# Optimization experiments

Hardware: AMD Instinct MI355X
Metric: run time of the kernel (lower is better)

Reference implementation:

```python
import jax, jax.numpy as jnp
import numpy as np

ATTN = 128

def _gelu(x):
    return jax.nn.gelu(x, approximate=False)

def _mlp3(x, W1, b1, W2, b2, W3, b3):
    h = _gelu(x @ W1.T + b1)
    h = _gelu(h @ W2.T + b2)
    return h @ W3.T + b3

def setup_inputs() -> dict:
    key = jax.random.key(0)
    ks = jax.random.split(key, 32)
    B, K, M, C = 128, 64, 2048, 32
    QD, AD, H = 128, 128, 256
    s = 0.02
    d = {}
    d['g'] = jax.random.normal(ks[0], (B, K, 3), dtype=jnp.float32)
    d['query'] = jax.random.normal(ks[1], (M, QD), dtype=jnp.float32) * s
    d['qW'] = jax.random.normal(ks[2], (AD, QD), dtype=jnp.float32) * s
    d['qb'] = jnp.zeros((AD,), jnp.float32)
    d['kW'] = jax.random.normal(ks[3], (AD, 1), dtype=jnp.float32) * s
    d['kb'] = jnp.zeros((AD,), jnp.float32)
    # global_mlp: K -> H -> H -> H
    d['gm_W1'] = jax.random.normal(ks[4], (H, K), dtype=jnp.float32) * s
    d['gm_b1'] = jnp.zeros((H,), jnp.float32)
    d['gm_W2'] = jax.random.normal(ks[5], (H, H), dtype=jnp.float32) * s
    d['gm_b2'] = jnp.zeros((H,), jnp.float32)
    d['gm_W3'] = jax.random.normal(ks[6], (H, H), dtype=jnp.float32) * s
    d['gm_b3'] = jnp.zeros((H,), jnp.float32)
    # point_mlp: (H+QD+1) -> H -> H -> H
    d['pm_W1'] = jax.random.normal(ks[7], (H, H + QD + 1), dtype=jnp.float32) * s
    d['pm_b1'] = jnp.zeros((H,), jnp.float32)
    d['pm_W2'] = jax.random.normal(ks[8], (H, H), dtype=jnp.float32) * s
    d['pm_b2'] = jnp.zeros((H,), jnp.float32)
    d['pm_W3'] = jax.random.normal(ks[9], (H, H), dtype=jnp.float32) * s
    d['pm_b3'] = jnp.zeros((H,), jnp.float32)
    d['tW'] = jax.random.normal(ks[10], (C, H), dtype=jnp.float32) * s
    d['tb'] = jnp.zeros((C,), jnp.float32)
    d['wW'] = jax.random.normal(ks[11], (1, H), dtype=jnp.float32) * s
    d['wb'] = jnp.zeros((1,), jnp.float32)
    d['cW'] = jax.random.normal(ks[12], (1, H), dtype=jnp.float32) * s
    d['cb'] = jnp.zeros((1,), jnp.float32)
    return d

def reference(g, query, qW, qb, kW, kb,
              gm_W1, gm_b1, gm_W2, gm_b2, gm_W3, gm_b3,
              pm_W1, pm_b1, pm_W2, pm_b2, pm_W3, pm_b3,
              tW, tb, wW, wb, cW, cb):
    B, K, _ = g.shape
    M = query.shape[0]
    inv = jnp.linalg.norm(g, axis=-1)                    # (B,K)
    Q = query @ qW.T + qb                                # (M,AD)
    Kk = inv[..., None] * kW[:, 0] + kb                  # (B,K,AD) Linear(1->AD)
    scores = jnp.einsum('md,bkd->bmk', Q, Kk) / jnp.sqrt(jnp.float32(Q.shape[-1]))
    A = jax.nn.softmax(scores, axis=-1)                  # (B,M,K)
    y = jnp.einsum('bmk,bkd->bmd', A, g)                 # (B,M,3)
    global_s = _mlp3(inv, gm_W1, gm_b1, gm_W2, gm_b2, gm_W3, gm_b3)  # (B,H)
    attended_inv = jnp.einsum('bmk,bk->bm', A, inv)      # (B,M)
    s_in = jnp.concatenate([
        jnp.broadcast_to(global_s[:, None, :], (B, M, global_s.shape[-1])),
        jnp.broadcast_to(query[None], (B, M, query.shape[-1])),
        attended_inv[..., None],
    ], axis=-1)                                          # (B,M,H+QD+1)
    s = _mlp3(s_in, pm_W1, pm_b1, pm_W2, pm_b2, pm_W3, pm_b3)  # (B,M,H)
    type_logits = s @ tW.T + tb                          # (B,M,C)
    weight_logits = (s @ wW.T + wb)[..., 0]              # (B,M)
    gate = jnp.clip(jax.nn.sigmoid(s @ cW.T + cb), 0.0, 1.0)  # (B,M,1)
    y = y * gate
    return (y, type_logits, weight_logits)
```

## Files before the change

kernel.cpp:

```cpp
#include <hip/hip_runtime.h>
#include <hip/hip_bf16.h>
#include <math.h>


typedef __attribute__((ext_vector_type(8))) short short8;
typedef __attribute__((ext_vector_type(4))) float f32x4;
typedef __attribute__((ext_vector_type(16))) float f32x16;

__device__ __forceinline__ unsigned short bf16_rne(float f){
    union { float f; unsigned u; } v; v.f = f;
    return (unsigned short)((v.u + 0x7FFFu + ((v.u >> 16) & 1u)) >> 16);
}
__device__ __forceinline__ unsigned pk_bf16(float a, float b){
    float2 t; t.x = a; t.y = b;
    __hip_bfloat162 h = __float22bfloat162_rn(t);
    union { __hip_bfloat162 h; unsigned u; } cv; cv.h = h;
    return cv.u;
}
__device__ __forceinline__ short8 cvt8_f4(const float* __restrict__ p){
    float4 a = *(const float4*)p;
    float4 b = *(const float4*)(p + 4);
    short8 s;
    s[0]=(short)bf16_rne(a.x); s[1]=(short)bf16_rne(a.y);
    s[2]=(short)bf16_rne(a.z); s[3]=(short)bf16_rne(a.w);
    s[4]=(short)bf16_rne(b.x); s[5]=(short)bf16_rne(b.y);
    s[6]=(short)bf16_rne(b.z); s[7]=(short)bf16_rne(b.w);
    return s;
}

__device__ __forceinline__ float gelu_f(float x){
    float z  = x * 0.70710678118654752f;
    float az = fabsf(z);
    float t  = __builtin_amdgcn_rcpf(1.0f + 0.3275911f * az);
    float p  = t*(0.254829592f + t*(-0.284496736f + t*(1.421413741f + t*(-1.453152027f + t*1.061405429f))));
    float e  = __expf(-az*az);
    float er = copysignf(1.0f - p*e, z);
    return 0.5f * x * (1.0f + er);
}
__device__ __forceinline__ float gelu_poly(float x){
    float t = x*x;
    float p = fmaf(t, -2.9761905e-3f, 2.5e-2f);
    p = fmaf(t, p, -0.16666667f);
    p = fmaf(t, p, 1.0f);
    float Phi = fmaf(x*p, 0.39894228f, 0.5f);
    Phi = fminf(fmaxf(Phi, 0.0f), 1.0f);
    return x * Phi;
}

__global__ __launch_bounds__(256)
void k_prep(const float* __restrict__ g, const float* __restrict__ qW,
            const float* __restrict__ qb, const float* __restrict__ kW,
            const float* __restrict__ query, const float* __restrict__ pmW1,
            const float* __restrict__ pmb1,
            const float* __restrict__ pmW2, const float* __restrict__ pmW3,
            const float* __restrict__ pmb3,
            const float* __restrict__ gmW1, const float* __restrict__ gmb1,
            const float* __restrict__ gmW2, const float* __restrict__ gmb2,
            const float* __restrict__ gmW3, const float* __restrict__ gmb3,
            const float* __restrict__ tW, const float* __restrict__ tb,
            const float* __restrict__ wW, const float* __restrict__ wb,
            const float* __restrict__ cW, const float* __restrict__ cb,
            float* __restrict__ invg, float* __restrict__ ag,
            float* __restrict__ u1g, float* __restrict__ u2g,
            unsigned short* __restrict__ w2b, unsigned short* __restrict__ wheadb,
            float* __restrict__ bheadg, float* __restrict__ w385g) {
    __shared__ __align__(16) unsigned char smem[87040];
    const int bid = blockIdx.x, tid = threadIdx.x;
    const int w = tid >> 6, lane = tid & 63, q = lane >> 4, ln = lane & 15;

    if (bid < 32) {
        int idx = bid*256 + tid;
        const float* p = g + idx*3;
        invg[idx] = sqrtf(p[0]*p[0] + p[1]*p[1] + p[2]*p[2]);
    } else if (bid < 96) {
        int o = (bid - 32)*1024 + tid*4;
        float4 x = *(const float4*)&pmW2[o];
        union { unsigned short u[4]; uint2 v; } r;
        r.u[0] = bf16_rne(x.x); r.u[1] = bf16_rne(x.y);
        r.u[2] = bf16_rne(x.z); r.u[3] = bf16_rne(x.w);
        *(uint2*)&w2b[o] = r.v;
    } else if (bid < 130) {
        float* hw = (float*)smem;
        int c = bid - 96;
        const float* src = (c < 32) ? (tW + c*256) : ((c == 32) ? wW : cW);
        hw[tid] = src[tid];
        __syncthreads();
        float acc = 0.f;
        for (int j = 0; j < 256; ++j) acc += hw[j] * pmW3[j*256 + tid];
        wheadb[c*256 + tid] = bf16_rne(acc);
        if (tid == 0) {
            float bacc = (c < 32) ? tb[c] : ((c == 32) ? wb[0] : cb[0]);
            for (int j = 0; j < 256; ++j) bacc += hw[j] * pmb3[j];
            bheadg[c] = bacc;
        }
    } else if (bid == 130) {
        w385g[tid] = pmW1[tid*385 + 384];
    } else if (bid < 139) {
        float* kws = (float*)smem;
        float* vs  = kws + 128;
        float* red = vs  + 128;
        if (tid < 128) kws[tid] = kW[tid];
        __syncthreads();
        if (tid < 128) {
            float acc = 0.f;
            for (int d = 0; d < 128; ++d) acc += qW[d*128 + tid] * kws[d];
            vs[tid] = acc;
            red[tid] = qb[tid] * kws[tid];
        }
        __syncthreads();
        float s0 = 0.f;
        #pragma unroll 8
        for (int i = 0; i < 128; ++i) s0 += red[i];
        int m = (bid - 131)*256 + tid;
        const float4* qp = (const float4*)(query + m*128);
        float acc = s0;
        #pragma unroll 8
        for (int e4 = 0; e4 < 32; ++e4) {
            float4 qv = qp[e4];
            acc += qv.x*vs[e4*4] + qv.y*vs[e4*4+1] + qv.z*vs[e4*4+2] + qv.w*vs[e4*4+3];
        }
        ag[m] = acc * 0.08838834764831845f;
    } else if (bid < 141) {
        unsigned short* invA = (unsigned short*)smem;
        unsigned short* hA   = (unsigned short*)(smem + 9216);
        unsigned short* hB   = (unsigned short*)(smem + 43008);
        const int b0 = (bid - 139)*64;
        for (int i = tid; i < 4096; i += 256) {
            int r = i >> 6, k = i & 63;
            const float* p = g + ((size_t)(b0 + r)*64 + k)*3;
            invA[r*72 + k] = bf16_rne(sqrtf(p[0]*p[0] + p[1]*p[1] + p[2]*p[2]));
        }
        __syncthreads();

        f32x4 acc[4][4];
        #pragma unroll
        for (int mt = 0; mt < 4; ++mt)
            #pragma unroll
            for (int nt = 0; nt < 4; ++nt) acc[mt][nt] = (f32x4){0.f,0.f,0.f,0.f};
        #pragma unroll
        for (int kk = 0; kk < 2; ++kk) {
            const int kc = kk*32 + q*8;
            short8 af[4], bf_[4];
            #pragma unroll
            for (int mt = 0; mt < 4; ++mt) af[mt] = *(const short8*)&invA[(mt*16 + ln)*72 + kc];
            #pragma unroll
            for (int nt = 0; nt < 4; ++nt) bf_[nt] = cvt8_f4(gmW1 + (w*64 + nt*16 + ln)*64 + kc);
            #pragma unroll
            for (int mt = 0; mt < 4; ++mt)
                #pragma unroll
                for (int nt = 0; nt < 4; ++nt)
                    acc[mt][nt] = __builtin_amdgcn_mfma_f32_16x16x32_bf16(af[mt], bf_[nt], acc[mt][nt], 0, 0, 0);
        }
        #pragma unroll
        for (int mt = 0; mt < 4; ++mt)
            #pragma unroll
            for (int nt = 0; nt < 4; ++nt) {
                const int n = w*64 + nt*16 + ln;
                const float bb = gmb1[n];
                #pragma unroll
                for (int rg = 0; rg < 4; ++rg)
                    hA[(mt*16 + q*4 + rg)*264 + n] = bf16_rne(gelu_f(acc[mt][nt][rg] + bb));
            }
        __syncthreads();
        #pragma unroll
        for (int mt = 0; mt < 4; ++mt)
            #pragma unroll
            for (int nt = 0; nt < 4; ++nt) acc[mt][nt] = (f32x4){0.f,0.f,0.f,0.f};
        for (int kk = 0; kk < 8; ++kk) {
            const int kc = kk*32 + q*8;
            short8 af[4], bf_[4];
            #pragma unroll
            for (int mt = 0; mt < 4; ++mt) af[mt] = *(const short8*)&hA[(mt*16 + ln)*264 + kc];
            #pragma unroll
            for (int nt = 0; nt < 4; ++nt) bf_[nt] = cvt8_f4(gmW2 + (w*64 + nt*16 + ln)*256 + kc);
            #pragma unroll
            for (int mt = 0; mt < 4; ++mt)
                #pragma unroll
                for (int nt = 0; nt < 4; ++nt)
                    acc[mt][nt] = __builtin_amdgcn_mfma_f32_16x16x32_bf16(af[mt], bf_[nt], acc[mt][nt], 0, 0, 0);
        }
        __syncthreads();
        #pragma unroll
        for (int mt = 0; mt < 4; ++mt)
            #pragma unroll
            for (int nt = 0; nt < 4; ++nt) {
                const int n = w*64 + nt*16 + ln;
                const float bb = gmb2[n];
                #pragma unroll
                for (int rg = 0; rg < 4; ++rg)
                    hB[(mt*16 + q*4 + rg)*264 + n] = bf16_rne(gelu_f(acc[mt][nt][rg] + bb));
            }
        __syncthreads();
        #pragma unroll
        for (int mt = 0; mt < 4; ++mt)
            #pragma unroll
            for (int nt = 0; nt < 4; ++nt) acc[mt][nt] = (f32x4){0.f,0.f,0.f,0.f};
        for (int kk = 0; kk < 8; ++kk) {
            const int kc = kk*32 + q*8;
            short8 af[4], bf_[4];
            #pragma unroll
            for (int mt = 0; mt < 4; ++mt) af[mt] = *(const short8*)&hB[(mt*16 + ln)*264 + kc];
            #pragma unroll
            for (int nt = 0; nt < 4; ++nt) bf_[nt] = cvt8_f4(gmW3 + (w*64 + nt*16 + ln)*256 + kc);
            #pragma unroll
            for (int mt = 0; mt < 4; ++mt)
                #pragma unroll
                for (int nt = 0; nt < 4; ++nt)
                    acc[mt][nt] = __builtin_amdgcn_mfma_f32_16x16x32_bf16(af[mt], bf_[nt], acc[mt][nt], 0, 0, 0);
        }
        __syncthreads();
        #pragma unroll
        for (int mt = 0; mt < 4; ++mt)
            #pragma unroll
            for (int nt = 0; nt < 4; ++nt) {
                const int n = w*64 + nt*16 + ln;
                const float bb = gmb3[n];
                #pragma unroll
                for (int rg = 0; rg < 4; ++rg)
                    hA[(mt*16 + q*4 + rg)*264 + n] = bf16_rne(acc[mt][nt][rg] + bb);
            }
        unsigned short* w1s = (unsigned short*)(smem + 43008);
        #pragma unroll
        for (int mt = 0; mt < 4; ++mt)
            #pragma unroll
            for (int nt = 0; nt < 4; ++nt) acc[mt][nt] = (f32x4){0.f,0.f,0.f,0.f};
        for (int chunk = 0; chunk < 4; ++chunk) {
            __syncthreads();
            for (int i = tid; i < 256*64; i += 256) {
                int n = i >> 6, c = i & 63;
                w1s[n*72 + c] = bf16_rne(pmW1[(size_t)n*385 + chunk*64 + c]);
            }
            __syncthreads();
            #pragma unroll
            for (int kk2 = 0; kk2 < 2; ++kk2) {
                const int kl = kk2*32 + q*8;
                const int kg = chunk*64 + kl;
                short8 af[4], bf_[4];
                #pragma unroll
                for (int mt = 0; mt < 4; ++mt) af[mt] = *(const short8*)&hA[(mt*16 + ln)*264 + kg];
                #pragma unroll
                for (int nt = 0; nt < 4; ++nt) bf_[nt] = *(const short8*)&w1s[(w*64 + nt*16 + ln)*72 + kl];
                #pragma unroll
                for (int mt = 0; mt < 4; ++mt)
                    #pragma unroll
                    for (int nt = 0; nt < 4; ++nt)
                        acc[mt][nt] = __builtin_amdgcn_mfma_f32_16x16x32_bf16(af[mt], bf_[nt], acc[mt][nt], 0, 0, 0);
            }
        }
        #pragma unroll
        for (int mt = 0; mt < 4; ++mt)
            #pragma unroll
            for (int nt = 0; nt < 4; ++nt) {
                const int n = w*64 + nt*16 + ln;
                const float bb = pmb1[n];
                #pragma unroll
                for (int rg = 0; rg < 4; ++rg)
                    u1g[(size_t)(b0 + mt*16 + q*4 + rg)*256 + n] = acc[mt][nt][rg] + bb;
            }
    } else {
        unsigned short* qs = (unsigned short*)smem;
        unsigned short* wsd = (unsigned short*)(smem + 17408);
        const int m0 = (bid - 141)*64;
        for (int i = tid; i < 64*128; i += 256) {
            int r = i >> 7, c = i & 127;
            qs[r*136 + c] = bf16_rne(query[(size_t)(m0 + r)*128 + c]);
        }
        for (int i = tid; i < 256*128; i += 256) {
            int n = i >> 7, c = i & 127;
            wsd[n*136 + c] = bf16_rne(pmW1[(size_t)n*385 + 256 + c]);
        }
        __syncthreads();
        f32x4 acc[4][4];
        #pragma unroll
        for (int mt = 0; mt < 4; ++mt)
            #pragma unroll
            for (int nt = 0; nt < 4; ++nt) acc[mt][nt] = (f32x4){0.f,0.f,0.f,0.f};
        #pragma unroll
        for (int kk = 0; kk < 4; ++kk) {
            const int kc = kk*32 + q*8;
            short8 af[4], bf_[4];
            #pragma unroll
            for (int mt = 0; mt < 4; ++mt) af[mt] = *(const short8*)&qs[(mt*16 + ln)*136 + kc];
            #pragma unroll
            for (int nt = 0; nt < 4; ++nt) bf_[nt] = *(const short8*)&wsd[(w*64 + nt*16 + ln)*136 + kc];
            #pragma unroll
            for (int mt = 0; mt < 4; ++mt)
                #pragma unroll
                for (int nt = 0; nt < 4; ++nt)
                    acc[mt][nt] = __builtin_amdgcn_mfma_f32_16x16x32_bf16(af[mt], bf_[nt], acc[mt][nt], 0, 0, 0);
        }
        #pragma unroll
        for (int mt = 0; mt < 4; ++mt)
            #pragma unroll
            for (int nt = 0; nt < 4; ++nt) {
                const int n = w*64 + nt*16 + ln;
                #pragma unroll
                for (int rg = 0; rg < 4; ++rg)
                    u2g[(size_t)(m0 + mt*16 + q*4 + rg)*256 + n] = acc[mt][nt][rg];
            }
    }
}

__global__ __launch_bounds__(256, 6)
void k_main(const float* __restrict__ g,
            const float* __restrict__ invg, const float* __restrict__ ag,
            const float* __restrict__ u1g, const float* __restrict__ u2g,
            const float* __restrict__ w385g, const float* __restrict__ pmb2,
            const unsigned short* __restrict__ w2b, const unsigned short* __restrict__ wheadb,
            const float* __restrict__ bheadg, float* __restrict__ out) {
    __shared__ __align__(16) unsigned short hb[32*264];
    __shared__ __align__(16) float u1s[256], w385s[256], pmb2s[256];
    __shared__ float invs[64], gsl[192], ainv_s[32], y0s[96];

    const int tid = threadIdx.x;
    const int bid = blockIdx.x;
    const int b  = bid >> 6;
    const int m0 = (bid & 63) << 5;

    if (tid < 64)  invs[tid] = invg[b*64 + tid];
    if (tid < 192) gsl[tid]  = g[b*192 + tid];
    u1s[tid]   = u1g[b*256 + tid];
    w385s[tid] = w385g[tid];
    pmb2s[tid] = pmb2[tid];
    __syncthreads();

    {
        const int r = tid >> 3, sub = tid & 7;
        const float am = ag[m0 + r];
        const int kb = sub * 8;
        float mx = -1e30f;
        #pragma unroll
        for (int i = 0; i < 8; ++i) mx = fmaxf(mx, invs[kb + i] * am);
        #pragma unroll
        for (int d = 1; d < 8; d <<= 1) mx = fmaxf(mx, __shfl_xor(mx, d, 64));
        float den = 0.f, ai = 0.f, y0 = 0.f, y1 = 0.f, y2 = 0.f;
        #pragma unroll
        for (int i = 0; i < 8; ++i) {
            const int k = kb + i;
            const float iv = invs[k];
            const float e = __expf(iv * am - mx);
            den += e; ai += e * iv;
            y0 += e * gsl[k*3+0]; y1 += e * gsl[k*3+1]; y2 += e * gsl[k*3+2];
        }
        #pragma unroll
        for (int d = 1; d < 8; d <<= 1) {
            den += __shfl_xor(den, d, 64);
            ai  += __shfl_xor(ai , d, 64);
            y0  += __shfl_xor(y0 , d, 64);
            y1  += __shfl_xor(y1 , d, 64);
            y2  += __shfl_xor(y2 , d, 64);
        }
        if (sub == 0) {
            const float id = 1.0f / den;
            ainv_s[r] = ai * id;
            y0s[r*3+0] = y0*id; y0s[r*3+1] = y1*id; y0s[r*3+2] = y2*id;
        }
    }
    __syncthreads();

    const int w = tid >> 6, lane = tid & 63;
    const int q = lane >> 4, ln = lane & 15;
    const int h5 = lane >> 5, m31 = lane & 31;

    const unsigned short* w2p = w2b + (size_t)(w*64 + m31)*256 + h5*8;
    short8 acur0 = *(const short8*)(w2p);
    short8 acur1 = *(const short8*)(w2p + 32*256);

    {
        const int ln16 = tid & 15, rbase = tid >> 4;
        #pragma unroll
        for (int rr = 0; rr < 2; ++rr) {
            const int r = rr*16 + rbase;
            const float aiv = ainv_s[r];
            const float* u2p = u2g + (size_t)(m0 + r)*256;
            #pragma unroll
            for (int k = 0; k < 4; ++k) {
                const int c = ln16*4 + k*64;
                float4 x  = *(const float4*)&u2p[c];
                float4 uv = *(const float4*)&u1s[c];
                float4 wv = *(const float4*)&w385s[c];
                float g0 = gelu_poly(x.x + uv.x + aiv*wv.x);
                float g1 = gelu_poly(x.y + uv.y + aiv*wv.y);
                float g2 = gelu_poly(x.z + uv.z + aiv*wv.z);
                float g3 = gelu_poly(x.w + uv.w + aiv*wv.w);
                uint2 pk; pk.x = pk_bf16(g0, g1); pk.y = pk_bf16(g2, g3);
                *(uint2*)&hb[r*264 + c] = pk;
            }
        }
    }
    __syncthreads();

    f32x16 acc2[2];
    #pragma unroll
    for (int a = 0; a < 2; ++a)
        #pragma unroll
        for (int i = 0; i < 16; ++i) acc2[a][i] = 0.f;

    {
        short8 anxt0, anxt1;
        #pragma unroll
        for (int kk = 0; kk < 16; ++kk) {
            if (kk < 15) {
                anxt0 = *(const short8*)(w2p + (kk+1)*16);
                anxt1 = *(const short8*)(w2p + 32*256 + (kk+1)*16);
            }
            const int kc = kk*16 + h5*8;
            short8 b0 = *(const short8*)&hb[m31*264 + kc];
            acc2[0] = __builtin_amdgcn_mfma_f32_32x32x16_bf16(acur0, b0, acc2[0], 0, 0, 0);
            acc2[1] = __builtin_amdgcn_mfma_f32_32x32x16_bf16(acur1, b0, acc2[1], 0, 0, 0);
            acur0 = anxt0; acur1 = anxt1;
        }
    }
    __syncthreads();

    #pragma unroll
    for (int a = 0; a < 2; ++a) {
        #pragma unroll
        for (int gg = 0; gg < 4; ++gg) {
            const int n0 = w*64 + a*32 + gg*8 + h5*4;
            const float4 bb4 = *(const float4*)&pmb2s[n0];
            float h0 = gelu_poly(acc2[a][gg*4+0] + bb4.x);
            float h1 = gelu_poly(acc2[a][gg*4+1] + bb4.y);
            float h2 = gelu_poly(acc2[a][gg*4+2] + bb4.z);
            float h3 = gelu_poly(acc2[a][gg*4+3] + bb4.w);
            uint2 pk2; pk2.x = pk_bf16(h0, h1); pk2.y = pk_bf16(h2, h3);
            *(uint2*)&hb[m31*264 + n0] = pk2;
        }
    }

    const int cb2 = (ln < 2) ? (32 + ln) : 33;
    const unsigned short* whp = wheadb + q*8;
    const bool evenw = ((w & 1) == 0);
    short8 wf0, wf1, wf2;
    if (evenw) {
        wf0 = *(const short8*)(whp +  ln      *256);
        wf1 = *(const short8*)(whp + (16 + ln)*256);
    } else {
        wf2 = *(const short8*)(whp +  cb2     *256);
    }
    __syncthreads();

    const int rr = (w >> 1)*16 + ln;
    f32x4 accA0 = {0.f,0.f,0.f,0.f}, accA1 = {0.f,0.f,0.f,0.f}, accB = {0.f,0.f,0.f,0.f};
    #pragma unroll
    for (int kk = 0; kk < 8; ++kk) {
        short8 wn0, wn1, wn2;
        if (kk < 7) {
            if (evenw) {
                wn0 = *(const short8*)(whp +  ln      *256 + (kk+1)*32);
                wn1 = *(const short8*)(whp + (16 + ln)*256 + (kk+1)*32);
            } else {
                wn2 = *(const short8*)(whp +  cb2     *256 + (kk+1)*32);
            }
        }
        short8 bh = *(const short8*)&hb[rr*264 + kk*32 + q*8];
        if (evenw) {
            accA0 = __builtin_amdgcn_mfma_f32_16x16x32_bf16(wf0, bh, accA0, 0, 0, 0);
            accA1 = __builtin_amdgcn_mfma_f32_16x16x32_bf16(wf1, bh, accA1, 0, 0, 0);
            wf0 = wn0; wf1 = wn1;
        } else {
            accB  = __builtin_amdgcn_mfma_f32_16x16x32_bf16(wf2, bh, accB , 0, 0, 0);
            wf2 = wn2;
        }
    }
    {
        const size_t row = (size_t)b*2048 + m0 + rr;
        const int c0 = q*4;
        if (evenw) {
            f32x4 r0 = accA0 + *(const f32x4*)&bheadg[c0];
            f32x4 r1 = accA1 + *(const f32x4*)&bheadg[16 + c0];
            *(f32x4*)&out[786432 + row*32 + c0]      = r0;
            *(f32x4*)&out[786432 + row*32 + 16 + c0] = r1;
        } else if (q == 0) {
            out[9175040 + row] = accB[0] + bheadg[32];
            float gv = accB[1] + bheadg[33];
            float gt = 1.0f / (1.0f + __expf(-gv));
            gt = fminf(fmaxf(gt, 0.0f), 1.0f);
            float* yo = out + row*3;
            yo[0] = y0s[rr*3+0] * gt;
            yo[1] = y0s[rr*3+1] * gt;
            yo[2] = y0s[rr*3+2] * gt;
        }
    }
}

extern "C" void kernel_launch(void* const* d_in, const int* in_sizes, int n_in,
                              void* d_out, int out_size, void* d_ws, size_t ws_size,
                              hipStream_t stream) {
    const float* g     = (const float*)d_in[0];
    const float* query = (const float*)d_in[1];
    const float* qW    = (const float*)d_in[2];
    const float* qb    = (const float*)d_in[3];
    const float* kW    = (const float*)d_in[4];
    const float* gmW1  = (const float*)d_in[6];
    const float* gmb1  = (const float*)d_in[7];
    const float* gmW2  = (const float*)d_in[8];
    const float* gmb2  = (const float*)d_in[9];
    const float* gmW3  = (const float*)d_in[10];
    const float* gmb3  = (const float*)d_in[11];
    const float* pmW1  = (const float*)d_in[12];
    const float* pmb1  = (const float*)d_in[13];
    const float* pmW2  = (const float*)d_in[14];
    const float* pmb2  = (const float*)d_in[15];
    const float* pmW3  = (const float*)d_in[16];
    const float* pmb3  = (const float*)d_in[17];
    const float* tW    = (const float*)d_in[18];
    const float* tb    = (const float*)d_in[19];
    const float* wW    = (const float*)d_in[20];
    const float* wb    = (const float*)d_in[21];
    const float* cW    = (const float*)d_in[22];
    const float* cb    = (const float*)d_in[23];
    float* out = (float*)d_out;

    float* ws    = (float*)d_ws;
    float* invg  = ws;
    float* ag    = ws + 8192;
    float* u1g   = ws + 10240;
    float* w385g = ws + 43008;
    float* bheadg= ws + 43264;
    unsigned short* w2b    = (unsigned short*)(ws + 43328);
    unsigned short* wheadb = (unsigned short*)(ws + 76096);
    float* u2g   = ws + 80448;

    hipLaunchKernelGGL(k_prep, dim3(173), dim3(256), 0, stream,
                       g, qW, qb, kW, query, pmW1, pmb1, pmW2, pmW3, pmb3,
                       gmW1, gmb1, gmW2, gmb2, gmW3, gmb3,
                       tW, tb, wW, wb, cW, cb,
                       invg, ag, u1g, u2g, w2b, wheadb, bheadg, w385g);
    hipLaunchKernelGGL(k_main, dim3(8192), dim3(256), 0, stream,
                       g, invg, ag, u1g, u2g, w385g, pmb2,
                       w2b, wheadb, bheadg, out);
}
```

Baseline: 314.9 us.

## Make k_main persistent per batch half with W2 resident in LDS

The main kernel now launches 256 blocks of 512 threads. Each block handles one batch element's half of the M rows and loops over 32 tiles of 32 rows. The full bf16 W2 matrix (256x256) is loaded into LDS once per block instead of being streamed from global memory for every 32-row tile. The next tile's u2 rows are prefetched into registers, and the head GEMMs are redistributed over 6 waves. The trade-offs are roughly 135KB of LDS per block, which forces one block per CU, only 256 blocks for the whole GPU, and a serial per-tile loop with several barriers per iteration.

```diff
diff --git a/kernel.cpp b/kernel.cpp
--- a/kernel.cpp
+++ b/kernel.cpp
@@ -301,60 +301,48 @@
     }
 }
 
-__global__ __launch_bounds__(256, 6)
+__global__ __launch_bounds__(512)
 void k_main(const float* __restrict__ g,
             const float* __restrict__ invg, const float* __restrict__ ag,
             const float* __restrict__ u1g, const float* __restrict__ u2g,
             const float* __restrict__ w385g, const float* __restrict__ pmb2,
             const unsigned short* __restrict__ w2b, const unsigned short* __restrict__ wheadb,
             const float* __restrict__ bheadg, float* __restrict__ out) {
+    __shared__ __align__(16) unsigned short w2s[256*264];
     __shared__ __align__(16) unsigned short hb[32*264];
-    __shared__ __align__(16) float u1s[256], w385s[256], pmb2s[256];
-    __shared__ float invs[64], gsl[192], ainv_s[32], y0s[96];
+    __shared__ __align__(16) float u1s[256];
+    __shared__ __align__(16) float w385s[256];
+    __shared__ __align__(16) float pmb2s[256];
+    __shared__ __align__(16) float bheads[36];
+    __shared__ float invs[64], gsl[192], y0s[96];
 
     const int tid = threadIdx.x;
     const int bid = blockIdx.x;
-    const int b  = bid >> 6;
-    const int m0 = (bid & 63) << 5;
+    const int b   = bid >> 1;
+    const int mbase = (bid & 1) << 10;
 
     if (tid < 64)  invs[tid] = invg[b*64 + tid];
     if (tid < 192) gsl[tid]  = g[b*192 + tid];
-    u1s[tid]   = u1g[b*256 + tid];
-    w385s[tid] = w385g[tid];
-    pmb2s[tid] = pmb2[tid];
-    __syncthreads();
-
+    if (tid < 256) {
+        u1s[tid]   = u1g[b*256 + tid];
+        w385s[tid] = w385g[tid];
+        pmb2s[tid] = pmb2[tid];
+    }
+    if (tid < 34) bheads[tid] = bheadg[tid];
+
+    const int r32 = tid >> 4;
+    const int cb  = (tid & 15) << 2;
+    float4 u2r[4];
     {
-        const int r = tid >> 3, sub = tid & 7;
-        const float am = ag[m0 + r];
-        const int kb = sub * 8;
-        float mx = -1e30f;
-        #pragma unroll
-        for (int i = 0; i < 8; ++i) mx = fmaxf(mx, invs[kb + i] * am);
-        #pragma unroll
-        for (int d = 1; d < 8; d <<= 1) mx = fmaxf(mx, __shfl_xor(mx, d, 64));
-        float den = 0.f, ai = 0.f, y0 = 0.f, y1 = 0.f, y2 = 0.f;
-        #pragma unroll
-        for (int i = 0; i < 8; ++i) {
-            const int k = kb + i;
-            const float iv = invs[k];
-            const float e = __expf(iv * am - mx);
-            den += e; ai += e * iv;
-            y0 += e * gsl[k*3+0]; y1 += e * gsl[k*3+1]; y2 += e * gsl[k*3+2];
-        }
-        #pragma unroll
-        for (int d = 1; d < 8; d <<= 1) {
-            den += __shfl_xor(den, d, 64);
-            ai  += __shfl_xor(ai , d, 64);
-            y0  += __shfl_xor(y0 , d, 64);
-            y1  += __shfl_xor(y1 , d, 64);
-            y2  += __shfl_xor(y2 , d, 64);
-        }
-        if (sub == 0) {
-            const float id = 1.0f / den;
-            ainv_s[r] = ai * id;
-            y0s[r*3+0] = y0*id; y0s[r*3+1] = y1*id; y0s[r*3+2] = y2*id;
-        }
+        const float* p = u2g + (size_t)(mbase + r32)*256 + cb;
+        #pragma unroll
+        for (int j = 0; j < 4; ++j) u2r[j] = *(const float4*)(p + j*64);
+    }
+    #pragma unroll
+    for (int j = 0; j < 16; ++j) {
+        int idx = tid + j*512;
+        int n = idx >> 5, c = (idx & 31) << 3;
+        *(short8*)&w2s[n*264 + c] = *(const short8*)&w2b[idx*8];
     }
     __syncthreads();
 
@@ -362,21 +350,43 @@
     const int q = lane >> 4, ln = lane & 15;
     const int h5 = lane >> 5, m31 = lane & 31;
 
-    const unsigned short* w2p = w2b + (size_t)(w*64 + m31)*256 + h5*8;
-    short8 acur0 = *(const short8*)(w2p);
-    short8 acur1 = *(const short8*)(w2p + 32*256);
-
-    {
-        const int ln16 = tid & 15, rbase = tid >> 4;
-        #pragma unroll
-        for (int rr = 0; rr < 2; ++rr) {
-            const int r = rr*16 + rbase;
-            const float aiv = ainv_s[r];
-            const float* u2p = u2g + (size_t)(m0 + r)*256;
-            #pragma unroll
-            for (int k = 0; k < 4; ++k) {
-                const int c = ln16*4 + k*64;
-                float4 x  = *(const float4*)&u2p[c];
+    for (int t = 0; t < 32; ++t) {
+        const int m0 = mbase + t*32;
+
+        {
+            const float am = ag[m0 + r32];
+            const int kb = (tid & 15) * 4;
+            float mx = -1e30f;
+            #pragma unroll
+            for (int i = 0; i < 4; ++i) mx = fmaxf(mx, invs[kb + i] * am);
+            #pragma unroll
+            for (int d = 1; d < 16; d <<= 1) mx = fmaxf(mx, __shfl_xor(mx, d, 64));
+            float den = 0.f, ai = 0.f, y0 = 0.f, y1 = 0.f, y2 = 0.f;
+            #pragma unroll
+            for (int i = 0; i < 4; ++i) {
+                const int k = kb + i;
+                const float iv = invs[k];
+                const float e = __expf(iv * am - mx);
+                den += e; ai += e * iv;
+                y0 += e * gsl[k*3+0]; y1 += e * gsl[k*3+1]; y2 += e * gsl[k*3+2];
+            }
+            #pragma unroll
+            for (int d = 1; d < 16; d <<= 1) {
+                den += __shfl_xor(den, d, 64);
+                ai  += __shfl_xor(ai , d, 64);
+                y0  += __shfl_xor(y0 , d, 64);
+                y1  += __shfl_xor(y1 , d, 64);
+                y2  += __shfl_xor(y2 , d, 64);
+            }
+            const float id = 1.0f / den;
+            const float aiv = ai * id;
+            if ((tid & 15) == 0) {
+                y0s[r32*3+0] = y0*id; y0s[r32*3+1] = y1*id; y0s[r32*3+2] = y2*id;
+            }
+            #pragma unroll
+            for (int j = 0; j < 4; ++j) {
+                const int c = cb + j*64;
+                float4 x  = u2r[j];
                 float4 uv = *(const float4*)&u1s[c];
                 float4 wv = *(const float4*)&w385s[c];
                 float g0 = gelu_poly(x.x + uv.x + aiv*wv.x);
@@ -384,103 +394,95 @@
                 float g2 = gelu_poly(x.z + uv.z + aiv*wv.z);
                 float g3 = gelu_poly(x.w + uv.w + aiv*wv.w);
                 uint2 pk; pk.x = pk_bf16(g0, g1); pk.y = pk_bf16(g2, g3);
-                *(uint2*)&hb[r*264 + c] = pk;
-            }
-        }
-    }
-    __syncthreads();
-
-    f32x16 acc2[2];
-    #pragma unroll
-    for (int a = 0; a < 2; ++a)
-        #pragma unroll
-        for (int i = 0; i < 16; ++i) acc2[a][i] = 0.f;
-
-    {
-        short8 anxt0, anxt1;
-        #pragma unroll
-        for (int kk = 0; kk < 16; ++kk) {
-            if (kk < 15) {
-                anxt0 = *(const short8*)(w2p + (kk+1)*16);
-                anxt1 = *(const short8*)(w2p + 32*256 + (kk+1)*16);
-            }
-            const int kc = kk*16 + h5*8;
-            short8 b0 = *(const short8*)&hb[m31*264 + kc];
-            acc2[0] = __builtin_amdgcn_mfma_f32_32x32x16_bf16(acur0, b0, acc2[0], 0, 0, 0);
-            acc2[1] = __builtin_amdgcn_mfma_f32_32x32x16_bf16(acur1, b0, acc2[1], 0, 0, 0);
-            acur0 = anxt0; acur1 = anxt1;
-        }
-    }
-    __syncthreads();
-
-    #pragma unroll
-    for (int a = 0; a < 2; ++a) {
+                *(uint2*)&hb[r32*264 + c] = pk;
+            }
+        }
+        if (t < 31) {
+            const float* p = u2g + (size_t)(m0 + 32 + r32)*256 + cb;
+            #pragma unroll
+            for (int j = 0; j < 4; ++j) u2r[j] = *(const float4*)(p + j*64);
+        }
+        __syncthreads();
+
+        f32x16 acc;
+        #pragma unroll
+        for (int i = 0; i < 16; ++i) acc[i] = 0.f;
+        {
+            const unsigned short* arow = &w2s[(w*32 + m31)*264 + h5*8];
+            const unsigned short* brow = &hb[m31*264 + h5*8];
+            short8 a0 = *(const short8*)arow;
+            short8 b0 = *(const short8*)brow;
+            #pragma unroll
+            for (int kk = 0; kk < 16; ++kk) {
+                short8 a1, b1;
+                if (kk < 15) {
+                    a1 = *(const short8*)(arow + (kk+1)*16);
+                    b1 = *(const short8*)(brow + (kk+1)*16);
+                }
+                acc = __builtin_amdgcn_mfma_f32_32x32x16_bf16(a0, b0, acc, 0, 0, 0);
+                a0 = a1; b0 = b1;
+            }
+        }
+        __syncthreads();
+
         #pragma unroll
         for (int gg = 0; gg < 4; ++gg) {
-            const int n0 = w*64 + a*32 + gg*8 + h5*4;
+            const int n0 = w*32 + gg*8 + h5*4;
             const float4 bb4 = *(const float4*)&pmb2s[n0];
-            float h0 = gelu_poly(acc2[a][gg*4+0] + bb4.x);
-            float h1 = gelu_poly(acc2[a][gg*4+1] + bb4.y);
-            float h2 = gelu_poly(acc2[a][gg*4+2] + bb4.z);
-            float h3 = gelu_poly(acc2[a][gg*4+3] + bb4.w);
+            float h0 = gelu_poly(acc[gg*4+0] + bb4.x);
+            float h1 = gelu_poly(acc[gg*4+1] + bb4.y);
+            float h2 = gelu_poly(acc[gg*4+2] + bb4.z);
+            float h3 = gelu_poly(acc[gg*4+3] + bb4.w);
             uint2 pk2; pk2.x = pk_bf16(h0, h1); pk2.y = pk_bf16(h2, h3);
             *(uint2*)&hb[m31*264 + n0] = pk2;
         }
-    }
-
-    const int cb2 = (ln < 2) ? (32 + ln) : 33;
-    const unsigned short* whp = wheadb + q*8;
-    const bool evenw = ((w & 1) == 0);
-    short8 wf0, wf1, wf2;
-    if (evenw) {
-        wf0 = *(const short8*)(whp +  ln      *256);
-        wf1 = *(const short8*)(whp + (16 + ln)*256);
-    } else {
-        wf2 = *(const short8*)(whp +  cb2     *256);
-    }
-    __syncthreads();
-
-    const int rr = (w >> 1)*16 + ln;
-    f32x4 accA0 = {0.f,0.f,0.f,0.f}, accA1 = {0.f,0.f,0.f,0.f}, accB = {0.f,0.f,0.f,0.f};
-    #pragma unroll
-    for (int kk = 0; kk < 8; ++kk) {
-        short8 wn0, wn1, wn2;
-        if (kk < 7) {
-            if (evenw) {
-                wn0 = *(const short8*)(whp +  ln      *256 + (kk+1)*32);
-                wn1 = *(const short8*)(whp + (16 + ln)*256 + (kk+1)*32);
-            } else {
-                wn2 = *(const short8*)(whp +  cb2     *256 + (kk+1)*32);
-            }
-        }
-        short8 bh = *(const short8*)&hb[rr*264 + kk*32 + q*8];
-        if (evenw) {
-            accA0 = __builtin_amdgcn_mfma_f32_16x16x32_bf16(wf0, bh, accA0, 0, 0, 0);
-            accA1 = __builtin_amdgcn_mfma_f32_16x16x32_bf16(wf1, bh, accA1, 0, 0, 0);
-            wf0 = wn0; wf1 = wn1;
-        } else {
-            accB  = __builtin_amdgcn_mfma_f32_16x16x32_bf16(wf2, bh, accB , 0, 0, 0);
-            wf2 = wn2;
-        }
-    }
-    {
-        const size_t row = (size_t)b*2048 + m0 + rr;
-        const int c0 = q*4;
-        if (evenw) {
-            f32x4 r0 = accA0 + *(const f32x4*)&bheadg[c0];
-            f32x4 r1 = accA1 + *(const f32x4*)&bheadg[16 + c0];
-            *(f32x4*)&out[786432 + row*32 + c0]      = r0;
-            *(f32x4*)&out[786432 + row*32 + 16 + c0] = r1;
-        } else if (q == 0) {
-            out[9175040 + row] = accB[0] + bheadg[32];
-            float gv = accB[1] + bheadg[33];
-            float gt = 1.0f / (1.0f + __expf(-gv));
-            gt = fminf(fmaxf(gt, 0.0f), 1.0f);
-            float* yo = out + row*3;
-            yo[0] = y0s[rr*3+0] * gt;
-            yo[1] = y0s[rr*3+1] * gt;
-            yo[2] = y0s[rr*3+2] * gt;
-        }
+        __syncthreads();
+
+        if (w < 4) {
+            const int rr = (w >> 1)*16 + ln;
+            const int ch = (w & 1)*16;
+            const unsigned short* whp = wheadb + (ch + ln)*256 + q*8;
+            f32x4 accA = {0.f,0.f,0.f,0.f};
+            short8 wf = *(const short8*)whp;
+            #pragma unroll
+            for (int kk = 0; kk < 8; ++kk) {
+                short8 wn;
+                if (kk < 7) wn = *(const short8*)(whp + (kk+1)*32);
+                short8 bh = *(const short8*)&hb[rr*264 + kk*32 + q*8];
+                accA = __builtin_amdgcn_mfma_f32_16x16x32_bf16(wf, bh, accA, 0, 0, 0);
+                wf = wn;
+            }
+            const size_t row = (size_t)b*2048 + m0 + rr;
+            const int c0 = ch + q*4;
+            f32x4 r0 = accA + *(const f32x4*)&bheads[c0];
+            *(f32x4*)&out[786432 + row*32 + c0] = r0;
+        } else if (w < 6) {
+            const int rr = (w - 4)*16 + ln;
+            const int cb2 = (ln < 2) ? (32 + ln) : 33;
+            const unsigned short* whp = wheadb + cb2*256 + q*8;
+            f32x4 accB = {0.f,0.f,0.f,0.f};
+            short8 wf = *(const short8*)whp;
+            #pragma unroll
+            for (int kk = 0; kk < 8; ++kk) {
+                short8 wn;
+                if (kk < 7) wn = *(const short8*)(whp + (kk+1)*32);
+                short8 bh = *(const short8*)&hb[rr*264 + kk*32 + q*8];
+                accB = __builtin_amdgcn_mfma_f32_16x16x32_bf16(wf, bh, accB, 0, 0, 0);
+                wf = wn;
+            }
+            if (q == 0) {
+                const size_t row = (size_t)b*2048 + m0 + rr;
+                out[9175040 + row] = accB[0] + bheads[32];
+                float gv = accB[1] + bheads[33];
+                float gt = 1.0f / (1.0f + __expf(-gv));
+                gt = fminf(fmaxf(gt, 0.0f), 1.0f);
+                float* yo = out + row*3;
+                yo[0] = y0s[rr*3+0] * gt;
+                yo[1] = y0s[rr*3+1] * gt;
+                yo[2] = y0s[rr*3+2] * gt;
+            }
+        }
+        __syncthreads();
     }
 }
 
@@ -527,7 +529,7 @@
                        gmW1, gmb1, gmW2, gmb2, gmW3, gmb3,
                        tW, tb, wW, wb, cW, cb,
                        invg, ag, u1g, u2g, w2b, wheadb, bheadg, w385g);
-    hipLaunchKernelGGL(k_main, dim3(8192), dim3(256), 0, stream,
+    hipLaunchKernelGGL(k_main, dim3(256), dim3(512), 0, stream,
                        g, invg, ag, u1g, u2g, w385g, pmb2,
                        w2b, wheadb, bheadg, out);
 }
```

After: 285.2 us. -9.4%, faster.
